# Kernel optimization log

Hardware: AMD Instinct MI355X
Metric: run time of the kernel (lower is better)

Reference implementation:

```python
import jax, jax.numpy as jnp
import numpy as np


def setup_inputs() -> dict:
    key = jax.random.key(0)
    ks = jax.random.split(key, 7)
    T, IN, H = 8192, 3000, 100
    s_ih = 1.0 / np.sqrt(H)
    return {
        "input_seq": jax.random.normal(ks[0], (T, IN), dtype=jnp.float32),
        "w_ih": jax.random.uniform(ks[1], (4 * H, IN), jnp.float32, -s_ih, s_ih),
        "w_hh": jax.random.uniform(ks[2], (4 * H, H), jnp.float32, -s_ih, s_ih),
        "b_ih": jax.random.uniform(ks[3], (4 * H,), jnp.float32, -s_ih, s_ih),
        "b_hh": jax.random.uniform(ks[4], (4 * H,), jnp.float32, -s_ih, s_ih),
        "w_lin": jax.random.uniform(ks[5], (1, H), jnp.float32, -s_ih, s_ih),
        "b_lin": jax.random.uniform(ks[6], (1,), jnp.float32, -s_ih, s_ih),
    }


def _lstm_scan(x_gates, w_hh, H):
    # x_gates: [T, 4H] precomputed input projections (incl. both biases)
    def step(carry, xg):
        h, c = carry
        g = xg + h @ w_hh.T  # [4H]
        i = jax.nn.sigmoid(g[:H])
        f = jax.nn.sigmoid(g[H:2 * H])
        gg = jnp.tanh(g[2 * H:3 * H])
        o = jax.nn.sigmoid(g[3 * H:])
        c = f * c + i * gg
        h = o * jnp.tanh(c)
        return (h, c), h

    h0 = jnp.zeros((H,), x_gates.dtype)
    c0 = jnp.zeros((H,), x_gates.dtype)
    _, hs = jax.lax.scan(step, (h0, c0), x_gates)
    return hs  # [T, H]


def reference(input_seq, w_ih, w_hh, b_ih, b_hh, w_lin, b_lin):
    H = w_hh.shape[1]
    # Fuse the per-timestep input GEMM into one big matmul (torch gate order i,f,g,o)
    x_gates = input_seq @ w_ih.T + b_ih + b_hh  # [T, 4H]
    hs = _lstm_scan(x_gates, w_hh, H)  # [T, H]
    preds = hs @ w_lin.T + b_lin  # [T, 1]
    return preds[-1]  # [1]
```

## Files before the change

kernel.cpp:

```cpp
#include <hip/hip_runtime.h>
#include <hip/hip_bf16.h>


#define GBM 128
#define GBN 128
#define GBK 16

typedef _Float16 h2_t __attribute__((ext_vector_type(2)));

__global__ __launch_bounds__(256) void gates_gemm(
    const float* __restrict__ A,
    const float* __restrict__ W,
    const float* __restrict__ bih,
    const float* __restrict__ bhh,
    float* __restrict__ XG,
    int T, int IN, int FH)
{
    __shared__ __align__(16) float As[GBK][GBM];
    __shared__ __align__(16) float Bs[GBK][GBN];
    const int bm = blockIdx.x * GBM;
    const int bn = blockIdx.y * GBN;
    const int tid = (int)threadIdx.x;
    const int tx = tid & 15, ty = tid >> 4;
    const int H = FH >> 2;

    float acc[8][8];
    #pragma unroll
    for (int i = 0; i < 8; ++i)
        #pragma unroll
        for (int j = 0; j < 8; ++j) acc[i][j] = 0.f;

    for (int k0 = 0; k0 < IN; k0 += GBK) {
        __syncthreads();
        #pragma unroll
        for (int q = 0; q < 2; ++q) {
            int idx = tid + q * 256;
            int row = idx >> 2;
            int kq  = (idx & 3) << 2;
            int gk  = k0 + kq;
            float4 av = make_float4(0.f, 0.f, 0.f, 0.f);
            float4 bv = make_float4(0.f, 0.f, 0.f, 0.f);
            if (gk < IN) {
                av = *(const float4*)&A[(size_t)(bm + row) * IN + gk];
                if (bn + row < FH)
                    bv = *(const float4*)&W[(size_t)(bn + row) * IN + gk];
            }
            As[kq + 0][row] = av.x; As[kq + 1][row] = av.y;
            As[kq + 2][row] = av.z; As[kq + 3][row] = av.w;
            Bs[kq + 0][row] = bv.x; Bs[kq + 1][row] = bv.y;
            Bs[kq + 2][row] = bv.z; Bs[kq + 3][row] = bv.w;
        }
        __syncthreads();
        #pragma unroll
        for (int kk = 0; kk < GBK; ++kk) {
            float4 a0 = *(const float4*)&As[kk][ty * 4];
            float4 a1 = *(const float4*)&As[kk][64 + ty * 4];
            float4 b0 = *(const float4*)&Bs[kk][tx * 4];
            float4 b1 = *(const float4*)&Bs[kk][64 + tx * 4];
            float am[8] = {a0.x, a0.y, a0.z, a0.w, a1.x, a1.y, a1.z, a1.w};
            float bn_[8] = {b0.x, b0.y, b0.z, b0.w, b1.x, b1.y, b1.z, b1.w};
            #pragma unroll
            for (int i = 0; i < 8; ++i)
                #pragma unroll
                for (int j = 0; j < 8; ++j)
                    acc[i][j] = fmaf(am[i], bn_[j], acc[i][j]);
        }
    }

    #pragma unroll
    for (int i = 0; i < 8; ++i) {
        int r = bm + ((i < 4) ? (ty * 4 + i) : (64 + ty * 4 + (i - 4)));
        #pragma unroll
        for (int j = 0; j < 8; ++j) {
            int cidx = bn + ((j < 4) ? (tx * 4 + j) : (64 + tx * 4 + (j - 4)));
            if (cidx < FH) {
                int pc = 4 * (cidx % H) + cidx / H;
                XG[(size_t)r * FH + pc] = acc[i][j] + bih[cidx] + bhh[cidx];
            }
        }
    }
}

__device__ __forceinline__ float pack_pair(const float* rp, int k) {
    float a = 0.f, b = 0.f;
    if (k < 100) { a = rp[k]; b = rp[k + 1]; }
    h2_t p = {(_Float16)a, (_Float16)b};
    return __builtin_bit_cast(float, p);
}

#define INITW(R, V) \
    asm volatile("v_mov_b32 v" #R ", %0" :: "v"(V) : "v" #R)

#define DD(A, W, Hr) "v_dot2_f32_f16 v" #A ", v" #W ", v" #Hr ", v" #A "\n\t"

#define VCLOB \
  "v96","v97","v98","v99","v100","v101","v102","v103","v104","v105","v106",\
  "v107","v108","v109","v110","v111","v112","v113","v114","v115","v116",\
  "v117","v118","v119","v120","v121","v122","v123","v124","v125","v126",\
  "v127","v128","v129","v130","v131","v132","v133","v134","v135","v136",\
  "v137","v138","v139","v140","v141","v142","v143","v144","v145","v146",\
  "v147","v148","v149","v150","v151","v152","v153","v154","v155","v156",\
  "v157","v158","v159","v160","v161","v162","v163","v164","v165","v166",\
  "v167","v168","v169","v170","v171","v172","v173","v174","v175","v176",\
  "v177","v178","v179","v180","v181","v182","v183","v184","v185","v186",\
  "v187","v188","v189","v190","v191","v192","v193","v194","v195","v196",\
  "v197","v198","v199","v200","v201","v202","v203","v204","v205","v206",\
  "v207","v208","v209","v210","v211","v212","v213","v214","v215","v216",\
  "v217","v218","v219","v220","v221","v222","v223","v224","v225","v226",\
  "v227","v228","v229","v230","v231","v232","v233","v234","v235","v236",\
  "v237","v238","v239","v240","v241","v242","v243","v244","v245","v246",\
  "v247","v248","v249","v250","v251","v252","v253","v254","v255"

#define BAR() asm volatile("s_waitcnt lgkmcnt(0)\n\ts_barrier" ::: "memory")

__global__ __launch_bounds__(256, 1) void lstm_scan_pinv(
    const float* __restrict__ XGp,
    const float* __restrict__ Whh,
    const float* __restrict__ wlin,
    const float* __restrict__ blin,
    float* __restrict__ out, int T)
{
    __shared__ __align__(16) _Float16 hbuf[2][104];
    __shared__ float hfin[100];
    const int tid    = (int)threadIdx.x;
    const int parity = tid & 1;
    const int p      = tid >> 1;
    const int pc     = (p < 100) ? p : 99;
    const bool act   = (parity == 0) && (p < 100);
    const float kk   = 1.f + (float)parity;

    const float* r0p = Whh + (size_t)(pc + parity * 200) * 100;
    const float* r1p = Whh + (size_t)(pc + 100 + parity * 200) * 100;

#define LW(j, R0, R1) { INITW(R0, pack_pair(r0p, 2*(j))); \
                        INITW(R1, pack_pair(r1p, 2*(j))); }
    LW(0,152,204)  LW(1,153,205)  LW(2,154,206)  LW(3,155,207)
    LW(4,156,208)  LW(5,157,209)  LW(6,158,210)  LW(7,159,211)
    LW(8,160,212)  LW(9,161,213)  LW(10,162,214) LW(11,163,215)
    LW(12,164,216) LW(13,165,217) LW(14,166,218) LW(15,167,219)
    LW(16,168,220) LW(17,169,221) LW(18,170,222) LW(19,171,223)
    LW(20,172,224) LW(21,173,225) LW(22,174,226) LW(23,175,227)
    LW(24,176,228) LW(25,177,229) LW(26,178,230) LW(27,179,231)
    LW(28,180,232) LW(29,181,233) LW(30,182,234) LW(31,183,235)
    LW(32,184,236) LW(33,185,237) LW(34,186,238) LW(35,187,239)
    LW(36,188,240) LW(37,189,241) LW(38,190,242) LW(39,191,243)
    LW(40,192,244) LW(41,193,245) LW(42,194,246) LW(43,195,247)
    LW(44,196,248) LW(45,197,249) LW(46,198,250) LW(47,199,251)
    LW(48,200,252) LW(49,201,253) LW(50,202,254) LW(51,203,255)
#undef LW

    if (tid < 104) { hbuf[0][tid] = (_Float16)0.f; hbuf[1][tid] = (_Float16)0.f; }

    const unsigned hb_base = (unsigned)(uintptr_t)&hbuf[0][0];

    const int xoff = 4 * pc + 2 * parity;
#define XR(i) (*(const float2*)(XGp + (size_t)((i) < T ? (i) : (T - 1)) * 400 + xoff))

    float2 xa = XR(0), xb = XR(1), xc = XR(2), xd = XR(3);

    float c = 0.f, hlast = 0.f;
    int cur = 0;
    BAR();

#define MATVEC(G0, G1, HB, X0, X1) \
    asm volatile( \
        "v_mov_b32 v148, %[x0]\n\t" \
        "v_mov_b32 v149, %[x1]\n\t" \
        "v_mov_b32 v150, 0\n\t" \
        "v_mov_b32 v151, 0\n\t" \
        "ds_read_b128 v[96:99], %[hb]\n\t" \
        "ds_read_b128 v[100:103], %[hb] offset:16\n\t" \
        "ds_read_b128 v[104:107], %[hb] offset:32\n\t" \
        "ds_read_b128 v[108:111], %[hb] offset:48\n\t" \
        "ds_read_b128 v[112:115], %[hb] offset:64\n\t" \
        "ds_read_b128 v[116:119], %[hb] offset:80\n\t" \
        "ds_read_b128 v[120:123], %[hb] offset:96\n\t" \
        "ds_read_b128 v[124:127], %[hb] offset:112\n\t" \
        "ds_read_b128 v[128:131], %[hb] offset:128\n\t" \
        "ds_read_b128 v[132:135], %[hb] offset:144\n\t" \
        "ds_read_b128 v[136:139], %[hb] offset:160\n\t" \
        "ds_read_b128 v[140:143], %[hb] offset:176\n\t" \
        "ds_read_b128 v[144:147], %[hb] offset:192\n\t" \
        "s_waitcnt lgkmcnt(9)\n\t" \
        DD(148,152,96)  DD(149,204,96)  DD(150,153,97)  DD(151,205,97) \
        DD(148,154,98)  DD(149,206,98)  DD(150,155,99)  DD(151,207,99) \
        DD(148,156,100) DD(149,208,100) DD(150,157,101) DD(151,209,101) \
        DD(148,158,102) DD(149,210,102) DD(150,159,103) DD(151,211,103) \
        DD(148,160,104) DD(149,212,104) DD(150,161,105) DD(151,213,105) \
        DD(148,162,106) DD(149,214,106) DD(150,163,107) DD(151,215,107) \
        DD(148,164,108) DD(149,216,108) DD(150,165,109) DD(151,217,109) \
        DD(148,166,110) DD(149,218,110) DD(150,167,111) DD(151,219,111) \
        "s_waitcnt lgkmcnt(5)\n\t" \
        DD(148,168,112) DD(149,220,112) DD(150,169,113) DD(151,221,113) \
        DD(148,170,114) DD(149,222,114) DD(150,171,115) DD(151,223,115) \
        DD(148,172,116) DD(149,224,116) DD(150,173,117) DD(151,225,117) \
        DD(148,174,118) DD(149,226,118) DD(150,175,119) DD(151,227,119) \
        DD(148,176,120) DD(149,228,120) DD(150,177,121) DD(151,229,121) \
        DD(148,178,122) DD(149,230,122) DD(150,179,123) DD(151,231,123) \
        DD(148,180,124) DD(149,232,124) DD(150,181,125) DD(151,233,125) \
        DD(148,182,126) DD(149,234,126) DD(150,183,127) DD(151,235,127) \
        "s_waitcnt lgkmcnt(1)\n\t" \
        DD(148,184,128) DD(149,236,128) DD(150,185,129) DD(151,237,129) \
        DD(148,186,130) DD(149,238,130) DD(150,187,131) DD(151,239,131) \
        DD(148,188,132) DD(149,240,132) DD(150,189,133) DD(151,241,133) \
        DD(148,190,134) DD(149,242,134) DD(150,191,135) DD(151,243,135) \
        DD(148,192,136) DD(149,244,136) DD(150,193,137) DD(151,245,137) \
        DD(148,194,138) DD(149,246,138) DD(150,195,139) DD(151,247,139) \
        DD(148,196,140) DD(149,248,140) DD(150,197,141) DD(151,249,141) \
        DD(148,198,142) DD(149,250,142) DD(150,199,143) DD(151,251,143) \
        "s_waitcnt lgkmcnt(0)\n\t" \
        DD(148,200,144) DD(149,252,144) DD(150,201,145) DD(151,253,145) \
        DD(148,202,146) DD(149,254,146) DD(150,203,147) DD(151,255,147) \
        "v_add_f32 %[g0], v148, v150\n\t" \
        "v_add_f32 %[g1], v149, v151" \
        : [g0]"=v"(G0), [g1]"=v"(G1) \
        : [hb]"v"(HB), [x0]"v"(X0), [x1]"v"(X1) \
        : VCLOB, "memory")

#define SUBSTEP(XP, TNEXT) { \
    unsigned hb_ = hb_base + (unsigned)(cur * 208); \
    float g0, g1; \
    MATVEC(g0, g1, hb_, XP.x, XP.y); \
    XP = XR(TNEXT);    \
     \
    float e0  = __expf(kk * g0); \
    float t0v = 1.f - kk * __builtin_amdgcn_rcpf(e0 + 1.f); \
    float e1  = __expf(-g1); \
    float t1v = __builtin_amdgcn_rcpf(1.f + e1);    \
    float rg_, ro_; \
    asm volatile("ds_swizzle_b32 %0, %2 offset:0x041F\n\t" \
                 "ds_swizzle_b32 %1, %3 offset:0x041F\n\t" \
                 "s_waitcnt lgkmcnt(0)" \
                 : "=&v"(rg_), "=&v"(ro_) : "v"(t0v), "v"(t1v)); \
    c = fmaf(t1v, c, t0v * rg_);           \
    float e2 = __expf(2.f * c); \
    float th = 1.f - 2.f * __builtin_amdgcn_rcpf(e2 + 1.f); \
    float hv_ = ro_ * th;                  \
    if (act) { hlast = hv_; hbuf[cur ^ 1][p] = (_Float16)hv_; } \
    BAR(); \
    cur ^= 1; }

    for (int t = 0; t < T; t += 4) {
        SUBSTEP(xa, t + 4)
        SUBSTEP(xb, t + 5)
        SUBSTEP(xc, t + 6)
        SUBSTEP(xd, t + 7)
    }
#undef SUBSTEP
#undef XR

    if (act) hfin[p] = hlast * wlin[p];
    __syncthreads();
    if (tid == 0) {
        float s = blin[0];
        for (int k = 0; k < 100; ++k) s += hfin[k];
        out[0] = s;
    }
}

extern "C" void kernel_launch(void* const* d_in, const int* in_sizes, int n_in,
                              void* d_out, int out_size, void* d_ws, size_t ws_size,
                              hipStream_t stream) {
    const float* input = (const float*)d_in[0];
    const float* w_ih  = (const float*)d_in[1];
    const float* w_hh  = (const float*)d_in[2];
    const float* b_ih  = (const float*)d_in[3];
    const float* b_hh  = (const float*)d_in[4];
    const float* w_lin = (const float*)d_in[5];
    const float* b_lin = (const float*)d_in[6];
    float* out = (float*)d_out;

    const int FH = in_sizes[3];
    const int IN = in_sizes[1] / FH;
    const int T  = in_sizes[0] / IN;

    float* xg = (float*)d_ws;

    dim3 grid((T + GBM - 1) / GBM, (FH + GBN - 1) / GBN);
    gates_gemm<<<grid, 256, 0, stream>>>(input, w_ih, b_ih, b_hh, xg, T, IN, FH);
    lstm_scan_pinv<<<1, 256, 0, stream>>>(xg, w_hh, w_lin, b_lin, out, T);
}
```

Before: 4.165 ms.

## Split recurrent matvec over K halves per thread pair, reduce with DPP

Each thread pair now owns one hidden unit with all four gates, and each thread of the pair covers half of the K dimension (50 columns) instead of half of the gate rows. Partial sums are combined with a DPP quad_perm add, which removes the ds_swizzle gate exchange and its LDS wait. Each thread now issues 100 dot2 per step instead of 104 and reads half as much h from LDS. In exchange, every thread evaluates all four activations redundantly, and h is stored with a padded split layout.

```diff
diff --git a/kernel.cpp b/kernel.cpp
--- a/kernel.cpp
+++ b/kernel.cpp
@@ -81,10 +81,15 @@
     }
 }
 
+__device__ __forceinline__ float sigmoid_fast(float x) {
+    return 1.f / (1.f + __expf(-x));
+}
+__device__ __forceinline__ float tanh_fast(float x) {
+    return 1.f - 2.f / (__expf(2.f * x) + 1.f);
+}
+
 __device__ __forceinline__ float pack_pair(const float* rp, int k) {
-    float a = 0.f, b = 0.f;
-    if (k < 100) { a = rp[k]; b = rp[k + 1]; }
-    h2_t p = {(_Float16)a, (_Float16)b};
+    h2_t p = {(_Float16)rp[k], (_Float16)rp[k + 1]};
     return __builtin_bit_cast(float, p);
 }
 
@@ -92,14 +97,15 @@
     asm volatile("v_mov_b32 v" #R ", %0" :: "v"(V) : "v" #R)
 
 #define DD(A, W, Hr) "v_dot2_f32_f16 v" #A ", v" #W ", v" #Hr ", v" #A "\n\t"
+
+#define Q4(H, WI, WF, WG, WO) \
+    DD(148,WI,H) DD(149,WF,H) DD(150,WG,H) DD(151,WO,H)
 
 #define VCLOB \
   "v96","v97","v98","v99","v100","v101","v102","v103","v104","v105","v106",\
   "v107","v108","v109","v110","v111","v112","v113","v114","v115","v116",\
-  "v117","v118","v119","v120","v121","v122","v123","v124","v125","v126",\
-  "v127","v128","v129","v130","v131","v132","v133","v134","v135","v136",\
-  "v137","v138","v139","v140","v141","v142","v143","v144","v145","v146",\
-  "v147","v148","v149","v150","v151","v152","v153","v154","v155","v156",\
+  "v117","v118","v119","v120",\
+  "v148","v149","v150","v151","v152","v153","v154","v155","v156",\
   "v157","v158","v159","v160","v161","v162","v163","v164","v165","v166",\
   "v167","v168","v169","v170","v171","v172","v173","v174","v175","v176",\
   "v177","v178","v179","v180","v181","v182","v183","v184","v185","v186",\
@@ -109,134 +115,117 @@
   "v217","v218","v219","v220","v221","v222","v223","v224","v225","v226",\
   "v227","v228","v229","v230","v231","v232","v233","v234","v235","v236",\
   "v237","v238","v239","v240","v241","v242","v243","v244","v245","v246",\
-  "v247","v248","v249","v250","v251","v252","v253","v254","v255"
+  "v247","v248","v249","v250","v251"
 
 #define BAR() asm volatile("s_waitcnt lgkmcnt(0)\n\ts_barrier" ::: "memory")
 
-__global__ __launch_bounds__(256, 1) void lstm_scan_pinv(
+__global__ __launch_bounds__(256, 1) void lstm_scan_ksplit(
     const float* __restrict__ XGp,
     const float* __restrict__ Whh,
     const float* __restrict__ wlin,
     const float* __restrict__ blin,
     float* __restrict__ out, int T)
 {
-    __shared__ __align__(16) _Float16 hbuf[2][104];
+    __shared__ __align__(16) _Float16 hbuf[2][112];
     __shared__ float hfin[100];
-    const int tid    = (int)threadIdx.x;
-    const int parity = tid & 1;
-    const int p      = tid >> 1;
-    const int pc     = (p < 100) ? p : 99;
-    const bool act   = (parity == 0) && (p < 100);
-    const float kk   = 1.f + (float)parity;
-
-    const float* r0p = Whh + (size_t)(pc + parity * 200) * 100;
-    const float* r1p = Whh + (size_t)(pc + 100 + parity * 200) * 100;
-
-#define LW(j, R0, R1) { INITW(R0, pack_pair(r0p, 2*(j))); \
-                        INITW(R1, pack_pair(r1p, 2*(j))); }
-    LW(0,152,204)  LW(1,153,205)  LW(2,154,206)  LW(3,155,207)
-    LW(4,156,208)  LW(5,157,209)  LW(6,158,210)  LW(7,159,211)
-    LW(8,160,212)  LW(9,161,213)  LW(10,162,214) LW(11,163,215)
-    LW(12,164,216) LW(13,165,217) LW(14,166,218) LW(15,167,219)
-    LW(16,168,220) LW(17,169,221) LW(18,170,222) LW(19,171,223)
-    LW(20,172,224) LW(21,173,225) LW(22,174,226) LW(23,175,227)
-    LW(24,176,228) LW(25,177,229) LW(26,178,230) LW(27,179,231)
-    LW(28,180,232) LW(29,181,233) LW(30,182,234) LW(31,183,235)
-    LW(32,184,236) LW(33,185,237) LW(34,186,238) LW(35,187,239)
-    LW(36,188,240) LW(37,189,241) LW(38,190,242) LW(39,191,243)
-    LW(40,192,244) LW(41,193,245) LW(42,194,246) LW(43,195,247)
-    LW(44,196,248) LW(45,197,249) LW(46,198,250) LW(47,199,251)
-    LW(48,200,252) LW(49,201,253) LW(50,202,254) LW(51,203,255)
-#undef LW
-
-    if (tid < 104) { hbuf[0][tid] = (_Float16)0.f; hbuf[1][tid] = (_Float16)0.f; }
+    const int tid = (int)threadIdx.x;
+    const int ph  = tid & 1;
+    const int u   = tid >> 1;
+    const int uc  = (u < 100) ? u : 99;
+    const bool act = (ph == 0) && (u < 100);
+    const int ko  = 50 * ph;
+
+    const float* ri = Whh + (size_t)(uc)       * 100;
+    const float* rf = Whh + (size_t)(uc + 100) * 100;
+    const float* rg = Whh + (size_t)(uc + 200) * 100;
+    const float* ro = Whh + (size_t)(uc + 300) * 100;
+
+#define LWX(j, RI, RF, RG, RO) { \
+    INITW(RI, pack_pair(ri, ko + 2*(j))); \
+    INITW(RF, pack_pair(rf, ko + 2*(j))); \
+    INITW(RG, pack_pair(rg, ko + 2*(j))); \
+    INITW(RO, pack_pair(ro, ko + 2*(j))); }
+    LWX(0,152,177,202,227)  LWX(1,153,178,203,228)  LWX(2,154,179,204,229)
+    LWX(3,155,180,205,230)  LWX(4,156,181,206,231)  LWX(5,157,182,207,232)
+    LWX(6,158,183,208,233)  LWX(7,159,184,209,234)  LWX(8,160,185,210,235)
+    LWX(9,161,186,211,236)  LWX(10,162,187,212,237) LWX(11,163,188,213,238)
+    LWX(12,164,189,214,239) LWX(13,165,190,215,240) LWX(14,166,191,216,241)
+    LWX(15,167,192,217,242) LWX(16,168,193,218,243) LWX(17,169,194,219,244)
+    LWX(18,170,195,220,245) LWX(19,171,196,221,246) LWX(20,172,197,222,247)
+    LWX(21,173,198,223,248) LWX(22,174,199,224,249) LWX(23,175,200,225,250)
+    LWX(24,176,201,226,251)
+#undef LWX
+
+    if (tid < 112) { hbuf[0][tid] = (_Float16)0.f; hbuf[1][tid] = (_Float16)0.f; }
 
     const unsigned hb_base = (unsigned)(uintptr_t)&hbuf[0][0];
-
-    const int xoff = 4 * pc + 2 * parity;
-#define XR(i) (*(const float2*)(XGp + (size_t)((i) < T ? (i) : (T - 1)) * 400 + xoff))
-
-    float2 xa = XR(0), xb = XR(1), xc = XR(2), xd = XR(3);
+    const unsigned hb_par  = hb_base + (unsigned)(112 * ph);
+
+#define XR(i) (*(const float4*)(XGp + (size_t)((i) < T ? (i) : (T - 1)) * 400 + 4 * uc))
+
+    float4 xa = XR(0), xb = XR(1), xc = XR(2), xd = XR(3);
 
     float c = 0.f, hlast = 0.f;
     int cur = 0;
     BAR();
 
-#define MATVEC(G0, G1, HB, X0, X1) \
+#define MATVEC4(G0, G1, G2, G3, HB, X0, X1, X2, X3) \
     asm volatile( \
         "v_mov_b32 v148, %[x0]\n\t" \
         "v_mov_b32 v149, %[x1]\n\t" \
-        "v_mov_b32 v150, 0\n\t" \
-        "v_mov_b32 v151, 0\n\t" \
+        "v_mov_b32 v150, %[x2]\n\t" \
+        "v_mov_b32 v151, %[x3]\n\t" \
         "ds_read_b128 v[96:99], %[hb]\n\t" \
         "ds_read_b128 v[100:103], %[hb] offset:16\n\t" \
         "ds_read_b128 v[104:107], %[hb] offset:32\n\t" \
         "ds_read_b128 v[108:111], %[hb] offset:48\n\t" \
         "ds_read_b128 v[112:115], %[hb] offset:64\n\t" \
         "ds_read_b128 v[116:119], %[hb] offset:80\n\t" \
-        "ds_read_b128 v[120:123], %[hb] offset:96\n\t" \
-        "ds_read_b128 v[124:127], %[hb] offset:112\n\t" \
-        "ds_read_b128 v[128:131], %[hb] offset:128\n\t" \
-        "ds_read_b128 v[132:135], %[hb] offset:144\n\t" \
-        "ds_read_b128 v[136:139], %[hb] offset:160\n\t" \
-        "ds_read_b128 v[140:143], %[hb] offset:176\n\t" \
-        "ds_read_b128 v[144:147], %[hb] offset:192\n\t" \
-        "s_waitcnt lgkmcnt(9)\n\t" \
-        DD(148,152,96)  DD(149,204,96)  DD(150,153,97)  DD(151,205,97) \
-        DD(148,154,98)  DD(149,206,98)  DD(150,155,99)  DD(151,207,99) \
-        DD(148,156,100) DD(149,208,100) DD(150,157,101) DD(151,209,101) \
-        DD(148,158,102) DD(149,210,102) DD(150,159,103) DD(151,211,103) \
-        DD(148,160,104) DD(149,212,104) DD(150,161,105) DD(151,213,105) \
-        DD(148,162,106) DD(149,214,106) DD(150,163,107) DD(151,215,107) \
-        DD(148,164,108) DD(149,216,108) DD(150,165,109) DD(151,217,109) \
-        DD(148,166,110) DD(149,218,110) DD(150,167,111) DD(151,219,111) \
-        "s_waitcnt lgkmcnt(5)\n\t" \
-        DD(148,168,112) DD(149,220,112) DD(150,169,113) DD(151,221,113) \
-        DD(148,170,114) DD(149,222,114) DD(150,171,115) DD(151,223,115) \
-        DD(148,172,116) DD(149,224,116) DD(150,173,117) DD(151,225,117) \
-        DD(148,174,118) DD(149,226,118) DD(150,175,119) DD(151,227,119) \
-        DD(148,176,120) DD(149,228,120) DD(150,177,121) DD(151,229,121) \
-        DD(148,178,122) DD(149,230,122) DD(150,179,123) DD(151,231,123) \
-        DD(148,180,124) DD(149,232,124) DD(150,181,125) DD(151,233,125) \
-        DD(148,182,126) DD(149,234,126) DD(150,183,127) DD(151,235,127) \
-        "s_waitcnt lgkmcnt(1)\n\t" \
-        DD(148,184,128) DD(149,236,128) DD(150,185,129) DD(151,237,129) \
-        DD(148,186,130) DD(149,238,130) DD(150,187,131) DD(151,239,131) \
-        DD(148,188,132) DD(149,240,132) DD(150,189,133) DD(151,241,133) \
-        DD(148,190,134) DD(149,242,134) DD(150,191,135) DD(151,243,135) \
-        DD(148,192,136) DD(149,244,136) DD(150,193,137) DD(151,245,137) \
-        DD(148,194,138) DD(149,246,138) DD(150,195,139) DD(151,247,139) \
-        DD(148,196,140) DD(149,248,140) DD(150,197,141) DD(151,249,141) \
-        DD(148,198,142) DD(149,250,142) DD(150,199,143) DD(151,251,143) \
+        "ds_read_b32 v120, %[hb] offset:96\n\t" \
+        "s_waitcnt lgkmcnt(3)\n\t" \
+        Q4(96,152,177,202,227)   Q4(97,153,178,203,228) \
+        Q4(98,154,179,204,229)   Q4(99,155,180,205,230) \
+        Q4(100,156,181,206,231)  Q4(101,157,182,207,232) \
+        Q4(102,158,183,208,233)  Q4(103,159,184,209,234) \
+        Q4(104,160,185,210,235)  Q4(105,161,186,211,236) \
+        Q4(106,162,187,212,237)  Q4(107,163,188,213,238) \
+        Q4(108,164,189,214,239)  Q4(109,165,190,215,240) \
+        Q4(110,166,191,216,241)  Q4(111,167,192,217,242) \
         "s_waitcnt lgkmcnt(0)\n\t" \
-        DD(148,200,144) DD(149,252,144) DD(150,201,145) DD(151,253,145) \
-        DD(148,202,146) DD(149,254,146) DD(150,203,147) DD(151,255,147) \
-        "v_add_f32 %[g0], v148, v150\n\t" \
-        "v_add_f32 %[g1], v149, v151" \
-        : [g0]"=v"(G0), [g1]"=v"(G1) \
-        : [hb]"v"(HB), [x0]"v"(X0), [x1]"v"(X1) \
+        Q4(112,168,193,218,243)  Q4(113,169,194,219,244) \
+        Q4(114,170,195,220,245)  Q4(115,171,196,221,246) \
+        Q4(116,172,197,222,247)  Q4(117,173,198,223,248) \
+        Q4(118,174,199,224,249)  Q4(119,175,200,225,250) \
+        Q4(120,176,201,226,251) \
+        "s_nop 1\n\t" \
+        "v_add_f32 %[g0], v148, v148 quad_perm:[1,0,3,2] row_mask:0xf bank_mask:0xf\n\t" \
+        "v_add_f32 %[g1], v149, v149 quad_perm:[1,0,3,2] row_mask:0xf bank_mask:0xf\n\t" \
+        "v_add_f32 %[g2], v150, v150 quad_perm:[1,0,3,2] row_mask:0xf bank_mask:0xf\n\t" \
+        "v_add_f32 %[g3], v151, v151 quad_perm:[1,0,3,2] row_mask:0xf bank_mask:0xf" \
+        : [g0]"=v"(G0), [g1]"=v"(G1), [g2]"=v"(G2), [g3]"=v"(G3) \
+        : [hb]"v"(HB), [x0]"v"(X0), [x1]"v"(X1), [x2]"v"(X2), [x3]"v"(X3) \
         : VCLOB, "memory")
 
 #define SUBSTEP(XP, TNEXT) { \
-    unsigned hb_ = hb_base + (unsigned)(cur * 208); \
-    float g0, g1; \
-    MATVEC(g0, g1, hb_, XP.x, XP.y); \
+    unsigned hb_ = hb_par + (unsigned)(cur * 224); \
+    float x0_ = ph ? 0.f : XP.x; \
+    float x1_ = ph ? 0.f : XP.y; \
+    float x2_ = ph ? 0.f : XP.z; \
+    float x3_ = ph ? 0.f : XP.w; \
+    float g0, g1, g2, g3; \
+    MATVEC4(g0, g1, g2, g3, hb_, x0_, x1_, x2_, x3_); \
     XP = XR(TNEXT);    \
-     \
-    float e0  = __expf(kk * g0); \
-    float t0v = 1.f - kk * __builtin_amdgcn_rcpf(e0 + 1.f); \
-    float e1  = __expf(-g1); \
-    float t1v = __builtin_amdgcn_rcpf(1.f + e1);    \
-    float rg_, ro_; \
-    asm volatile("ds_swizzle_b32 %0, %2 offset:0x041F\n\t" \
-                 "ds_swizzle_b32 %1, %3 offset:0x041F\n\t" \
-                 "s_waitcnt lgkmcnt(0)" \
-                 : "=&v"(rg_), "=&v"(ro_) : "v"(t0v), "v"(t1v)); \
-    c = fmaf(t1v, c, t0v * rg_);           \
-    float e2 = __expf(2.f * c); \
-    float th = 1.f - 2.f * __builtin_amdgcn_rcpf(e2 + 1.f); \
-    float hv_ = ro_ * th;                  \
-    if (act) { hlast = hv_; hbuf[cur ^ 1][p] = (_Float16)hv_; } \
+    float iv = sigmoid_fast(g0); \
+    float fv = sigmoid_fast(g1); \
+    float gv = tanh_fast(g2); \
+    float ov = sigmoid_fast(g3); \
+    c = fmaf(fv, c, iv * gv); \
+    float hv_ = ov * tanh_fast(c); \
+    if (act) { \
+        hlast = hv_; \
+        int hidx = (u < 50) ? u : (u + 6);    \
+        hbuf[cur ^ 1][hidx] = (_Float16)hv_; \
+    } \
     BAR(); \
     cur ^= 1; }
 
@@ -249,7 +238,7 @@
 #undef SUBSTEP
 #undef XR
 
-    if (act) hfin[p] = hlast * wlin[p];
+    if (act) hfin[u] = hlast * wlin[u];
     __syncthreads();
     if (tid == 0) {
         float s = blin[0];
@@ -278,5 +267,5 @@
 
     dim3 grid((T + GBM - 1) / GBM, (FH + GBN - 1) / GBN);
     gates_gemm<<<grid, 256, 0, stream>>>(input, w_ih, b_ih, b_hh, xg, T, IN, FH);
-    lstm_scan_pinv<<<1, 256, 0, stream>>>(xg, w_hh, w_lin, b_lin, out, T);
-}
+    lstm_scan_ksplit<<<1, 256, 0, stream>>>(xg, w_hh, w_lin, b_lin, out, T);
+}
```

Result: slower. 4.654 ms (+11.7%).
